# Performance work log

Measured on AMD Instinct MI355X. Metric: run time of the kernel, lower is better.

Reference implementation:

```python
import jax, jax.numpy as jnp
import numpy as np

N, E, B, H, L, T = 50000, 800000, 1000, 256, 5, 128
BN_EPS = 1e-5

def _bn(x, g, b):
    # training-mode batchnorm over node axis, biased variance (torch semantics)
    mu = jnp.mean(x, axis=0)
    var = jnp.mean(jnp.square(x - mu), axis=0)
    return (x - mu) * jax.lax.rsqrt(var + BN_EPS) * g + b

def setup_inputs() -> dict:
    key = jax.random.key(0)
    ks = jax.random.split(key, 12)
    s = lambda fan: 1.0 / np.sqrt(fan)
    inp = {}
    inp["x_atom"] = jax.random.normal(ks[0], (N, 9), jnp.float32)
    inp["x_pe"] = jax.random.normal(ks[1], (N, 8), jnp.float32)
    inp["edge_index"] = jax.random.randint(ks[2], (2, E), 0, N, dtype=jnp.int64)
    inp["batch"] = jnp.sort(jax.random.randint(ks[3], (N,), 0, B, dtype=jnp.int64))
    inp["ae_w"] = jax.random.normal(ks[4], (9, H), jnp.float32) * s(9)
    inp["ae_b"] = jnp.zeros((H,), jnp.float32)
    inp["pe_w"] = jax.random.normal(ks[5], (8, H), jnp.float32) * s(8)
    inp["pe_b"] = jnp.zeros((H,), jnp.float32)
    inp["w1"] = jax.random.normal(ks[6], (L, H, H), jnp.float32) * s(H)
    inp["b1"] = jnp.zeros((L, H), jnp.float32)
    inp["g1"] = jnp.ones((L, H), jnp.float32)
    inp["be1"] = jnp.zeros((L, H), jnp.float32)
    inp["w2"] = jax.random.normal(ks[7], (L, H, H), jnp.float32) * s(H)
    inp["b2"] = jnp.zeros((L, H), jnp.float32)
    inp["bng"] = jnp.ones((L, H), jnp.float32)
    inp["bnb"] = jnp.zeros((L, H), jnp.float32)
    inp["cl1_w"] = jax.random.normal(ks[8], (H, H), jnp.float32) * s(H)
    inp["cl1_b"] = jnp.zeros((H,), jnp.float32)
    inp["clg"] = jnp.ones((H,), jnp.float32)
    inp["clb"] = jnp.zeros((H,), jnp.float32)
    inp["cl2_w"] = jax.random.normal(ks[9], (H, T), jnp.float32) * s(H)
    inp["cl2_b"] = jnp.zeros((T,), jnp.float32)
    return inp

def reference(x_atom, x_pe, edge_index, batch, ae_w, ae_b, pe_w, pe_b,
              w1, b1, g1, be1, w2, b2, bng, bnb,
              cl1_w, cl1_b, clg, clb, cl2_w, cl2_b):
    src, dst = edge_index[0], edge_index[1]
    h = x_atom @ ae_w + ae_b + x_pe @ pe_w + pe_b  # (N, H)
    for i in range(L):
        # GINConv (eps=0): (1+eps)*x + sum_{j in N(i)} x_j, then MLP
        agg = jax.ops.segment_sum(h[src], dst, num_segments=N)
        z = h + agg
        z = z @ w1[i] + b1[i]
        z = jax.nn.relu(_bn(z, g1[i], be1[i]))
        z = z @ w2[i] + b2[i]
        # outer BN + ReLU (dropout is identity in eval)
        h = jax.nn.relu(_bn(z, bng[i], bnb[i]))
    # global mean pool per graph
    sums = jax.ops.segment_sum(h, batch, num_segments=B)
    counts = jax.ops.segment_sum(jnp.ones((N,), h.dtype), batch, num_segments=B)
    pooled = sums / jnp.maximum(counts, 1.0)[:, None]  # (B, H)
    z = pooled @ cl1_w + cl1_b
    z = jax.nn.relu(_bn(z, clg, clb))
    logits = z @ cl2_w + cl2_b  # (B, T)
    return logits
```

## Files before the change

kernel.cpp:

```cpp
#include <hip/hip_runtime.h>
#include <hip/hip_bf16.h>
#include <stdint.h>

#define HH 256
#define BN_EPS 1e-5f
#define CHUNK 256
#define NSLOT 12

static inline int cdiv(int a, int b) { return (a + b - 1) / b; }

typedef _Float16 f16x8 __attribute__((ext_vector_type(8)));
typedef __attribute__((ext_vector_type(4))) float f32x4;

__device__ __forceinline__ unsigned short f2h(float f) {
    _Float16 h = (_Float16)f;
    unsigned short u;
    __builtin_memcpy(&u, &h, 2);
    return u;
}
__device__ __forceinline__ float h2f(unsigned short u) {
    _Float16 h;
    __builtin_memcpy(&h, &u, 2);
    return (float)h;
}

__device__ __forceinline__ void gload16(const void* g, void* lds) {
    __builtin_amdgcn_global_load_lds((const __attribute__((address_space(1))) unsigned int*)g,
                                     (__attribute__((address_space(3))) unsigned int*)lds, 16, 0, 0);
}

__device__ __forceinline__ void bn_derive(const float* __restrict__ stats, const float* __restrict__ g,
                                          const float* __restrict__ b, float invM, int c,
                                          float& sc, float& sh) {
    float mu = stats[c] * invM;
    float var = stats[HH + c] * invM - mu * mu;
    float rstd = rsqrtf(var + BN_EPS);
    sc = rstd * g[c];
    sh = b[c] - mu * sc;
}

__global__ void embed_kernel(const float* __restrict__ xa, const float* __restrict__ xp,
                             const float* __restrict__ aw, const float* __restrict__ ab,
                             const float* __restrict__ pw, const float* __restrict__ pb,
                             unsigned short* __restrict__ h, int N) {
    int n = blockIdx.x;
    int c = threadIdx.x;
    if (n >= N) return;
    float acc = ab[c] + pb[c];
#pragma unroll
    for (int k = 0; k < 9; ++k) acc += xa[n * 9 + k] * aw[k * HH + c];
#pragma unroll
    for (int k = 0; k < 8; ++k) acc += xp[n * 8 + k] * pw[k * HH + c];
    h[(size_t)n * HH + c] = f2h(acc);
}

__global__ void zero_int_kernel(int* __restrict__ p, int n) {
    int i = blockIdx.x * blockDim.x + threadIdx.x;
    if (i < n) p[i] = 0;
}

__global__ void hist_kernel(const int* __restrict__ ei, int* __restrict__ deg, int E) {
    int e = blockIdx.x * blockDim.x + threadIdx.x;
    if (e < E) atomicAdd(&deg[ei[(size_t)E + e]], 1);
}

__global__ void ps1_kernel(const int* __restrict__ deg, int* __restrict__ chunkSum, int N) {
    __shared__ int sm[CHUNK];
    int i = blockIdx.x * CHUNK + threadIdx.x;
    sm[threadIdx.x] = (i < N) ? deg[i] : 0;
    __syncthreads();
    for (int off = CHUNK / 2; off > 0; off >>= 1) {
        if (threadIdx.x < off) sm[threadIdx.x] += sm[threadIdx.x + off];
        __syncthreads();
    }
    if (threadIdx.x == 0) chunkSum[blockIdx.x] = sm[0];
}

__global__ void ps2_kernel(const int* __restrict__ chunkSum, int* __restrict__ chunkOff,
                           int nc, int* __restrict__ offs, int N, int E) {
    __shared__ int sm[CHUNK];
    int t = threadIdx.x;
    int own = (t < nc) ? chunkSum[t] : 0;
    sm[t] = own;
    for (int off = 1; off < CHUNK; off <<= 1) {
        __syncthreads();
        int v = (t >= off) ? sm[t - off] : 0;
        __syncthreads();
        sm[t] += v;
    }
    if (t < nc) chunkOff[t] = sm[t] - own;
    if (t == 0) offs[N] = E;
}

__global__ void ps3_kernel(const int* __restrict__ deg, const int* __restrict__ chunkOff,
                           int* __restrict__ offs, int* __restrict__ cursor, int N) {
    __shared__ int sm[CHUNK];
    int t = threadIdx.x;
    int i = blockIdx.x * CHUNK + t;
    int own = (i < N) ? deg[i] : 0;
    sm[t] = own;
    for (int off = 1; off < CHUNK; off <<= 1) {
        __syncthreads();
        int v = (t >= off) ? sm[t - off] : 0;
        __syncthreads();
        sm[t] += v;
    }
    if (i < N) {
        int o = chunkOff[blockIdx.x] + sm[t] - own;
        offs[i] = o;
        cursor[i] = o;
    }
}

__global__ void fill_kernel(const int* __restrict__ ei, int* __restrict__ cursor,
                            int* __restrict__ srcl, int E) {
    int e = blockIdx.x * blockDim.x + threadIdx.x;
    if (e >= E) return;
    int s = ei[e];
    int d = ei[(size_t)E + e];
    int pos = atomicAdd(&cursor[d], 1);
    srcl[pos] = s;
}

__global__ void transpose_w_kernel(const float* __restrict__ W1, const float* __restrict__ W2,
                                   unsigned short* __restrict__ Wt1, unsigned short* __restrict__ Wt2,
                                   int perSet) {
    __shared__ float tile[32][33];
    int id = blockIdx.x;
    const float* W = W1;
    unsigned short* Wt = Wt1;
    if (id >= perSet) { W = W2; Wt = Wt2; id -= perSet; }
    int mat = id >> 6, t = id & 63;
    int kt = (t >> 3) * 32, nt = (t & 7) * 32;
    const float* Wm = W + (size_t)mat * HH * HH;
    unsigned short* Wtm = Wt + (size_t)mat * HH * HH;
    int lx = threadIdx.x & 31, ly = threadIdx.x >> 5;
#pragma unroll
    for (int yy = 0; yy < 32; yy += 8)
        tile[ly + yy][lx] = Wm[(size_t)(kt + ly + yy) * HH + nt + lx];
    __syncthreads();
#pragma unroll
    for (int yy = 0; yy < 32; yy += 8)
        Wtm[(size_t)(nt + ly + yy) * HH + kt + lx] = f2h(tile[lx][ly + yy]);
}

__global__ void init_stats_kernel(float* __restrict__ stats) {
    int i = blockIdx.x * blockDim.x + threadIdx.x;
    int slot = i >> 9;
    if (slot < NSLOT) stats[(size_t)slot * 4 * HH + (i & 511)] = 0.f;
}

__global__ __launch_bounds__(256) void aggregate_fused_kernel(
        const unsigned short* __restrict__ h,
        const int* __restrict__ offs, const int* __restrict__ srcl,
        const float* __restrict__ stats, const float* __restrict__ gv,
        const float* __restrict__ bv, float invM,
        unsigned short* __restrict__ z, int N) {
    int n = blockIdx.x * 4 + (threadIdx.x >> 6);
    int l = threadIdx.x & 63;
    if (n >= N) return;
    int c = l * 4;
    const bool apply = (stats != nullptr);
    float sc0 = 1.f, sc1 = 1.f, sc2 = 1.f, sc3 = 1.f;
    float sh0 = 0.f, sh1 = 0.f, sh2 = 0.f, sh3 = 0.f;
    if (apply) {
        bn_derive(stats, gv, bv, invM, c + 0, sc0, sh0);
        bn_derive(stats, gv, bv, invM, c + 1, sc1, sh1);
        bn_derive(stats, gv, bv, invM, c + 2, sc2, sh2);
        bn_derive(stats, gv, bv, invM, c + 3, sc3, sh3);
    }

#define LOADT(row, r0, r1, r2, r3)                                      \
    {                                                                   \
        ushort4 v_ = *(const ushort4*)&h[(size_t)(row) * HH + c];       \
        r0 = h2f(v_.x); r1 = h2f(v_.y); r2 = h2f(v_.z); r3 = h2f(v_.w); \
        if (apply) {                                                    \
            r0 = fmaxf(r0 * sc0 + sh0, 0.f);                            \
            r1 = fmaxf(r1 * sc1 + sh1, 0.f);                            \
            r2 = fmaxf(r2 * sc2 + sh2, 0.f);                            \
            r3 = fmaxf(r3 * sc3 + sh3, 0.f);                            \
        }                                                               \
    }

    float a0, a1, a2, a3;
    LOADT(n, a0, a1, a2, a3);
    int s0 = offs[n], s1 = offs[n + 1];
    int j = s0;
    for (; j + 4 <= s1; j += 4) {
        int r0 = srcl[j], r1 = srcl[j + 1], r2 = srcl[j + 2], r3 = srcl[j + 3];
        float t0, t1, t2, t3, u0, u1, u2, u3;
        float p0, p1, p2, p3, q0, q1, q2, q3;
        LOADT(r0, t0, t1, t2, t3);
        LOADT(r1, u0, u1, u2, u3);
        LOADT(r2, p0, p1, p2, p3);
        LOADT(r3, q0, q1, q2, q3);
        a0 += (t0 + u0) + (p0 + q0);
        a1 += (t1 + u1) + (p1 + q1);
        a2 += (t2 + u2) + (p2 + q2);
        a3 += (t3 + u3) + (p3 + q3);
    }
    for (; j < s1; ++j) {
        float t0, t1, t2, t3;
        LOADT(srcl[j], t0, t1, t2, t3);
        a0 += t0; a1 += t1; a2 += t2; a3 += t3;
    }
#undef LOADT
    ushort4 o;
    o.x = f2h(a0); o.y = f2h(a1); o.z = f2h(a2); o.w = f2h(a3);
    *(ushort4*)&z[(size_t)n * HH + c] = o;
}

template <bool BN>
__global__ __launch_bounds__(256) void mfma_gemm_t(const unsigned short* __restrict__ A,
                                                   const unsigned short* __restrict__ Wt,
                                                   const float* __restrict__ bias,
                                                   unsigned short* __restrict__ C,
                                                   float* __restrict__ stats,
                                                   const float* __restrict__ bnstats,
                                                   const float* __restrict__ gv,
                                                   const float* __restrict__ bv,
                                                   float invM, int M) {
    __shared__ unsigned short sm[128 * 136];
    __shared__ __align__(16) _Float16 lsc[256];
    __shared__ __align__(16) _Float16 lsh[256];
    unsigned short* As = sm;
    unsigned short* Bs = sm + 128 * 64;
    int tid = threadIdx.x;
    int w = tid >> 6, l = tid & 63;
    int wr = w >> 1, wc = w & 1;
    int row0 = blockIdx.y * 128;
    int col0 = blockIdx.x * 128;
    int g = (l & 7) ^ (l >> 3);
    int srow = w * 8 + (l >> 3);

    if (BN) {
        float sc, sh;
        bn_derive(bnstats, gv, bv, invM, tid, sc, sh);
        lsc[tid] = (_Float16)sc;
        lsh[tid] = (_Float16)sh;
        __syncthreads();
    }

    f32x4 acc[4][4] = {};

    const unsigned short* AB = A + (size_t)row0 * HH;
    const unsigned short* WB = Wt + (size_t)col0 * HH;

    for (int k0 = 0; k0 < 256; k0 += 64) {
#pragma unroll
        for (int r = 0; r < 4; ++r) {
            int row = r * 32 + srow;
            size_t go = (size_t)row * HH + k0 + g * 8;
            int lo = (r * 32 + w * 8) * 64;
            gload16(AB + go, &As[lo]);
            gload16(WB + go, &Bs[lo]);
        }
        __syncthreads();
#pragma unroll
        for (int kh = 0; kh < 2; ++kh) {
            f16x8 af[4], bf[4];
            f16x8 scv, shv;
            if (BN) {
                int kb = k0 + (kh * 4 + (l >> 4)) * 8;
                scv = *(const f16x8*)&lsc[kb];
                shv = *(const f16x8*)&lsh[kb];
            }
#pragma unroll
            for (int m = 0; m < 4; ++m) {
                int rr = wr * 64 + m * 16 + (l & 15);
                int gs = (kh * 4 + (l >> 4)) ^ (rr & 7);
                af[m] = *(const f16x8*)&As[rr * 64 + gs * 8];
                if (BN) {
                    af[m] = af[m] * scv + shv;
                    af[m] = __builtin_elementwise_max(af[m], (f16x8)(_Float16)0);
                }
            }
#pragma unroll
            for (int n = 0; n < 4; ++n) {
                int rr = wc * 64 + n * 16 + (l & 15);
                int gs = (kh * 4 + (l >> 4)) ^ (rr & 7);
                bf[n] = *(const f16x8*)&Bs[rr * 64 + gs * 8];
            }
#pragma unroll
            for (int m = 0; m < 4; ++m)
#pragma unroll
                for (int n = 0; n < 4; ++n)
                    acc[m][n] = __builtin_amdgcn_mfma_f32_16x16x32_f16(af[m], bf[n], acc[m][n], 0, 0, 0);
        }
        __syncthreads();
    }

    int mvalid = M - row0;
#pragma unroll
    for (int n = 0; n < 4; ++n) {
        int colr = wc * 64 + n * 16 + (l & 15);
        float bvv = bias[col0 + colr];
        float s = 0.f, s2 = 0.f;
#pragma unroll
        for (int m = 0; m < 4; ++m) {
            int rb = wr * 64 + m * 16 + (l >> 4) * 4;
#pragma unroll
            for (int r = 0; r < 4; ++r) {
                float v = acc[m][n][r] + bvv;
                sm[(rb + r) * 136 + colr] = f2h(v);
                if (rb + r < mvalid) { s += v; s2 += v * v; }
            }
        }
        s += __shfl_xor(s, 16);   s += __shfl_xor(s, 32);
        s2 += __shfl_xor(s2, 16); s2 += __shfl_xor(s2, 32);
        if ((l >> 4) == 0) {
            atomicAdd(&stats[col0 + colr], s);
            atomicAdd(&stats[HH + col0 + colr], s2);
        }
    }
    __syncthreads();
#pragma unroll
    for (int i = 0; i < 8; ++i) {
        int ci = i * 256 + tid;
        int row = ci >> 4;
        int cq = (ci & 15) * 8;
        if (row0 + row < M) {
            uint4 v = *(const uint4*)&sm[row * 136 + cq];
            *(uint4*)&C[(size_t)(row0 + row) * HH + col0 + cq] = v;
        }
    }
}

__global__ void bn_stats_kernel(const float* __restrict__ X, int M, float* __restrict__ stats) {
    int c = threadIdx.x;
    int r0 = blockIdx.x * 128;
    int r1 = min(r0 + 128, M);
    float s = 0.f, s2 = 0.f;
    for (int r = r0; r < r1; ++r) {
        float v = X[(size_t)r * HH + c];
        s += v;
        s2 += v * v;
    }
    atomicAdd(&stats[c], s);
    atomicAdd(&stats[HH + c], s2);
}

__global__ void bn_finalize_kernel(float* __restrict__ stats, const float* __restrict__ g,
                                   const float* __restrict__ b, float invM) {
    int c = threadIdx.x;
    float sc, sh;
    bn_derive(stats, g, b, invM, c, sc, sh);
    stats[2 * HH + c] = sc;
    stats[3 * HH + c] = sh;
}

__global__ void bn_apply_relu_kernel(float* __restrict__ X, int n4, const float* __restrict__ stats) {
    int i = blockIdx.x * blockDim.x + threadIdx.x;
    int stride = gridDim.x * blockDim.x;
    for (; i < n4; i += stride) {
        int c4 = (i & 63) * 4;
        float4 v = ((float4*)X)[i];
        float4 sc = *(const float4*)&stats[2 * HH + c4];
        float4 sh = *(const float4*)&stats[3 * HH + c4];
        v.x = fmaxf(v.x * sc.x + sh.x, 0.f);
        v.y = fmaxf(v.y * sc.y + sh.y, 0.f);
        v.z = fmaxf(v.z * sc.z + sh.z, 0.f);
        v.w = fmaxf(v.w * sc.w + sh.w, 0.f);
        ((float4*)X)[i] = v;
    }
}

__global__ __launch_bounds__(256) void gemm_kernel(const float* __restrict__ A,
                                                   const float* __restrict__ W,
                                                   const float* __restrict__ bias,
                                                   float* __restrict__ C,
                                                   int M, int ldw) {
    __shared__ float Asm[64][33];
    __shared__ float Wsm[32][64];
    int tid = threadIdx.x;
    int tx = tid & 15, ty = tid >> 4;
    int row0 = blockIdx.x * 64;
    int col0 = blockIdx.y * 64;
    float acc[4][4] = {};

    for (int k0 = 0; k0 < 256; k0 += 32) {
#pragma unroll
        for (int t = 0; t < 2; ++t) {
            int s = tid + t * 256;
            int m = s >> 3;
            int kq = (s & 7) * 4;
            float4 v = make_float4(0.f, 0.f, 0.f, 0.f);
            if (row0 + m < M) v = *(const float4*)&A[(size_t)(row0 + m) * 256 + k0 + kq];
            Asm[m][kq + 0] = v.x; Asm[m][kq + 1] = v.y; Asm[m][kq + 2] = v.z; Asm[m][kq + 3] = v.w;
        }
#pragma unroll
        for (int t = 0; t < 2; ++t) {
            int s = tid + t * 256;
            int kk = s >> 4;
            int cq = (s & 15) * 4;
            *(float4*)&Wsm[kk][cq] = *(const float4*)&W[(size_t)(k0 + kk) * ldw + col0 + cq];
        }
        __syncthreads();
#pragma unroll
        for (int kk = 0; kk < 32; ++kk) {
            float a0 = Asm[ty * 4 + 0][kk];
            float a1 = Asm[ty * 4 + 1][kk];
            float a2 = Asm[ty * 4 + 2][kk];
            float a3 = Asm[ty * 4 + 3][kk];
            float4 wv = *(const float4*)&Wsm[kk][tx * 4];
            acc[0][0] += a0 * wv.x; acc[0][1] += a0 * wv.y; acc[0][2] += a0 * wv.z; acc[0][3] += a0 * wv.w;
            acc[1][0] += a1 * wv.x; acc[1][1] += a1 * wv.y; acc[1][2] += a1 * wv.z; acc[1][3] += a1 * wv.w;
            acc[2][0] += a2 * wv.x; acc[2][1] += a2 * wv.y; acc[2][2] += a2 * wv.z; acc[2][3] += a2 * wv.w;
            acc[3][0] += a3 * wv.x; acc[3][1] += a3 * wv.y; acc[3][2] += a3 * wv.z; acc[3][3] += a3 * wv.w;
        }
        __syncthreads();
    }

    float4 bvv = *(const float4*)&bias[col0 + tx * 4];
#pragma unroll
    for (int j = 0; j < 4; ++j) {
        int row = row0 + ty * 4 + j;
        if (row < M) {
            float4 o = make_float4(acc[j][0] + bvv.x, acc[j][1] + bvv.y,
                                   acc[j][2] + bvv.z, acc[j][3] + bvv.w);
            *(float4*)&C[(size_t)row * ldw + col0 + tx * 4] = o;
        }
    }
}

__device__ __forceinline__ int lbound(const int* a, int n, int v) {
    int lo = 0, hi = n;
    while (lo < hi) {
        int mid = (lo + hi) >> 1;
        if (a[mid] < v) lo = mid + 1; else hi = mid;
    }
    return lo;
}

__global__ void pool_fused_kernel(const unsigned short* __restrict__ Hm,
                                  const int* __restrict__ batch,
                                  const float* __restrict__ stats,
                                  const float* __restrict__ gv,
                                  const float* __restrict__ bv, float invM,
                                  int N, float* __restrict__ pooled) {
    int g = blockIdx.x;
    int c = threadIdx.x;
    int s = lbound(batch, N, g);
    int e = lbound(batch, N, g + 1);
    float sc, sh;
    bn_derive(stats, gv, bv, invM, c, sc, sh);
    float acc = 0.f;
    for (int r = s; r < e; ++r)
        acc += fmaxf(h2f(Hm[(size_t)r * HH + c]) * sc + sh, 0.f);
    pooled[(size_t)g * HH + c] = acc / (float)max(e - s, 1);
}

extern "C" void kernel_launch(void* const* d_in, const int* in_sizes, int n_in,
                              void* d_out, int out_size, void* d_ws, size_t ws_size,
                              hipStream_t stream) {
    const float* x_atom = (const float*)d_in[0];
    const float* x_pe   = (const float*)d_in[1];
    const int* ei       = (const int*)d_in[2];
    const int* batch    = (const int*)d_in[3];
    const float* ae_w = (const float*)d_in[4];
    const float* ae_b = (const float*)d_in[5];
    const float* pe_w = (const float*)d_in[6];
    const float* pe_b = (const float*)d_in[7];
    const float* w1  = (const float*)d_in[8];
    const float* b1  = (const float*)d_in[9];
    const float* g1  = (const float*)d_in[10];
    const float* be1 = (const float*)d_in[11];
    const float* w2  = (const float*)d_in[12];
    const float* b2  = (const float*)d_in[13];
    const float* bng = (const float*)d_in[14];
    const float* bnb = (const float*)d_in[15];
    const float* cl1_w = (const float*)d_in[16];
    const float* cl1_b = (const float*)d_in[17];
    const float* clg = (const float*)d_in[18];
    const float* clb = (const float*)d_in[19];
    const float* cl2_w = (const float*)d_in[20];
    const float* cl2_b = (const float*)d_in[21];

    const int N = in_sizes[3];
    const int E = in_sizes[2] / 2;
    const int T = in_sizes[21];
    const int B = out_size / T;
    const int Lnum = in_sizes[9] / HH;
    const int nc = cdiv(N, CHUNK);
    const int Npad = cdiv(N, 128) * 128;
    const size_t P = (size_t)Npad * HH;

    unsigned short* X = (unsigned short*)d_ws;
    unsigned short* Y = X + P;
    unsigned short* wt1 = Y + P;
    unsigned short* wt2 = wt1 + (size_t)Lnum * HH * HH;
    float* stats = (float*)(wt2 + (size_t)Lnum * HH * HH);
    float* pooled = stats + (size_t)NSLOT * 4 * HH;
    float* zc = pooled + (size_t)B * HH;
    int* deg = (int*)(zc + (size_t)B * HH);
    int* offs = deg + N;
    int* cursor = offs + N + 1;
    int* chunkSum = cursor + N;
    int* chunkOff = chunkSum + 256;
    int* srcl = chunkOff + 256;

    const int BH4 = B * (HH / 4);
    const float invN = 1.f / (float)N;

    zero_int_kernel<<<cdiv(N, 256), 256, 0, stream>>>(deg, N);
    hist_kernel<<<cdiv(E, 256), 256, 0, stream>>>(ei, deg, E);
    ps1_kernel<<<nc, CHUNK, 0, stream>>>(deg, chunkSum, N);
    ps2_kernel<<<1, CHUNK, 0, stream>>>(chunkSum, chunkOff, nc, offs, N, E);
    ps3_kernel<<<nc, CHUNK, 0, stream>>>(deg, chunkOff, offs, cursor, N);
    fill_kernel<<<cdiv(E, 256), 256, 0, stream>>>(ei, cursor, srcl, E);

    transpose_w_kernel<<<2 * Lnum * 64, 256, 0, stream>>>(w1, w2, wt1, wt2, Lnum * 64);

    init_stats_kernel<<<cdiv(NSLOT * 512, 256), 256, 0, stream>>>(stats);

    embed_kernel<<<N, HH, 0, stream>>>(x_atom, x_pe, ae_w, ae_b, pe_w, pe_b, X, N);

    dim3 mf_grid(2, cdiv(N, 128));

    unsigned short *in = X, *ot = Y;

    for (int i = 0; i < Lnum; ++i) {
        float* slot1 = stats + (size_t)(2 * i) * 4 * HH;
        float* slot2 = stats + (size_t)(2 * i + 1) * 4 * HH;
        const float* aggStats = (i == 0) ? nullptr : stats + (size_t)(2 * i - 1) * 4 * HH;
        const float* aggG = (i == 0) ? nullptr : bng + (size_t)(i - 1) * HH;
        const float* aggB = (i == 0) ? nullptr : bnb + (size_t)(i - 1) * HH;

        aggregate_fused_kernel<<<cdiv(N, 4), 256, 0, stream>>>(in, offs, srcl,
                                                               aggStats, aggG, aggB, invN, ot, N);

        mfma_gemm_t<false><<<mf_grid, 256, 0, stream>>>(ot, wt1 + (size_t)i * HH * HH,
                                                        b1 + (size_t)i * HH, in, slot1,
                                                        nullptr, nullptr, nullptr, 0.f, N);

        mfma_gemm_t<true><<<mf_grid, 256, 0, stream>>>(in, wt2 + (size_t)i * HH * HH,
                                                       b2 + (size_t)i * HH, ot, slot2,
                                                       slot1, g1 + (size_t)i * HH,
                                                       be1 + (size_t)i * HH, invN, N);

        unsigned short* t = in; in = ot; ot = t;
    }

    pool_fused_kernel<<<B, HH, 0, stream>>>(in, batch,
                                            stats + (size_t)(2 * Lnum - 1) * 4 * HH,
                                            bng + (size_t)(Lnum - 1) * HH,
                                            bnb + (size_t)(Lnum - 1) * HH, invN, N, pooled);

    float* slotC = stats + (size_t)10 * 4 * HH;
    dim3 cls_grid1(cdiv(B, 64), HH / 64);
    gemm_kernel<<<cls_grid1, 256, 0, stream>>>(pooled, cl1_w, cl1_b, zc, B, HH);
    bn_stats_kernel<<<cdiv(B, 128), HH, 0, stream>>>(zc, B, slotC);
    bn_finalize_kernel<<<1, HH, 0, stream>>>(slotC, clg, clb, 1.f / B);
    bn_apply_relu_kernel<<<min(2048, cdiv(BH4, 256)), 256, 0, stream>>>(zc, BH4, slotC);

    dim3 cls_grid2(cdiv(B, 64), T / 64);
    gemm_kernel<<<cls_grid2, 256, 0, stream>>>(zc, cl2_w, cl2_b, (float*)d_out, B, T);
}
```

Before: 1.018 ms.

## Remap GEMM block order for XCD locality, pre-reduce BN stats in LDS, merge init kernels

Result: faster. 888.6 us (-12.7%).

```diff
diff --git a/kernel.cpp b/kernel.cpp
--- a/kernel.cpp
+++ b/kernel.cpp
@@ -54,9 +54,13 @@
     h[(size_t)n * HH + c] = f2h(acc);
 }
 
-__global__ void zero_int_kernel(int* __restrict__ p, int n) {
+__global__ void setup_kernel(int* __restrict__ deg, int N, float* __restrict__ stats) {
     int i = blockIdx.x * blockDim.x + threadIdx.x;
-    if (i < n) p[i] = 0;
+    if (i < N) deg[i] = 0;
+    if (i < NSLOT * 512) {
+        int slot = i >> 9;
+        stats[(size_t)slot * 4 * HH + (i & 511)] = 0.f;
+    }
 }
 
 __global__ void hist_kernel(const int* __restrict__ ei, int* __restrict__ deg, int E) {
@@ -142,12 +146,6 @@
 #pragma unroll
     for (int yy = 0; yy < 32; yy += 8)
         Wtm[(size_t)(nt + ly + yy) * HH + kt + lx] = f2h(tile[lx][ly + yy]);
-}
-
-__global__ void init_stats_kernel(float* __restrict__ stats) {
-    int i = blockIdx.x * blockDim.x + threadIdx.x;
-    int slot = i >> 9;
-    if (slot < NSLOT) stats[(size_t)slot * 4 * HH + (i & 511)] = 0.f;
 }
 
 __global__ __launch_bounds__(256) void aggregate_fused_kernel(
@@ -223,13 +221,29 @@
     __shared__ unsigned short sm[128 * 136];
     __shared__ __align__(16) _Float16 lsc[256];
     __shared__ __align__(16) _Float16 lsh[256];
+    __shared__ float sred[256];
     unsigned short* As = sm;
     unsigned short* Bs = sm + 128 * 64;
     int tid = threadIdx.x;
     int w = tid >> 6, l = tid & 63;
     int wr = w >> 1, wc = w & 1;
-    int row0 = blockIdx.y * 128;
-    int col0 = blockIdx.x * 128;
+
+    int nRow = (M + 127) >> 7;
+    int fullIds = (nRow & ~7) * 2;
+    int id = blockIdx.x;
+    int p, cc;
+    if (id < fullIds) {
+        int gq = id >> 4, r = id & 15;
+        cc = r >> 3;
+        p = gq * 8 + (r & 7);
+    } else {
+        int t = id - fullIds;
+        p = (nRow & ~7) + (t >> 1);
+        cc = t & 1;
+    }
+    int row0 = p * 128;
+    int col0 = cc * 128;
+
     int g = (l & 7) ^ (l >> 3);
     int srow = w * 8 + (l >> 3);
 
@@ -291,6 +305,7 @@
     }
 
     int mvalid = M - row0;
+    float sv[4], s2v[4];
 #pragma unroll
     for (int n = 0; n < 4; ++n) {
         int colr = wc * 64 + n * 16 + (l & 15);
@@ -308,12 +323,26 @@
         }
         s += __shfl_xor(s, 16);   s += __shfl_xor(s, 32);
         s2 += __shfl_xor(s2, 16); s2 += __shfl_xor(s2, 32);
-        if ((l >> 4) == 0) {
-            atomicAdd(&stats[col0 + colr], s);
-            atomicAdd(&stats[HH + col0 + colr], s2);
+        sv[n] = s;
+        s2v[n] = s2;
+    }
+    if (wr == 1 && (l >> 4) == 0) {
+#pragma unroll
+        for (int n = 0; n < 4; ++n) {
+            int colr = wc * 64 + n * 16 + (l & 15);
+            sred[colr] = sv[n];
+            sred[128 + colr] = s2v[n];
         }
     }
     __syncthreads();
+    if (wr == 0 && (l >> 4) == 0) {
+#pragma unroll
+        for (int n = 0; n < 4; ++n) {
+            int colr = wc * 64 + n * 16 + (l & 15);
+            atomicAdd(&stats[col0 + colr], sv[n] + sred[colr]);
+            atomicAdd(&stats[HH + col0 + colr], s2v[n] + sred[128 + colr]);
+        }
+    }
 #pragma unroll
     for (int i = 0; i < 8; ++i) {
         int ci = i * 256 + tid;
@@ -502,7 +531,8 @@
     const int BH4 = B * (HH / 4);
     const float invN = 1.f / (float)N;
 
-    zero_int_kernel<<<cdiv(N, 256), 256, 0, stream>>>(deg, N);
+    setup_kernel<<<cdiv(max(N, NSLOT * 512), 256), 256, 0, stream>>>(deg, N, stats);
+
     hist_kernel<<<cdiv(E, 256), 256, 0, stream>>>(ei, deg, E);
     ps1_kernel<<<nc, CHUNK, 0, stream>>>(deg, chunkSum, N);
     ps2_kernel<<<1, CHUNK, 0, stream>>>(chunkSum, chunkOff, nc, offs, N, E);
@@ -511,11 +541,10 @@
 
     transpose_w_kernel<<<2 * Lnum * 64, 256, 0, stream>>>(w1, w2, wt1, wt2, Lnum * 64);
 
-    init_stats_kernel<<<cdiv(NSLOT * 512, 256), 256, 0, stream>>>(stats);
-
     embed_kernel<<<N, HH, 0, stream>>>(x_atom, x_pe, ae_w, ae_b, pe_w, pe_b, X, N);
 
-    dim3 mf_grid(2, cdiv(N, 128));
+    const int nRow = cdiv(N, 128);
+    const int mf_blocks = 2 * nRow;
 
     unsigned short *in = X, *ot = Y;
 
@@ -529,14 +558,14 @@
         aggregate_fused_kernel<<<cdiv(N, 4), 256, 0, stream>>>(in, offs, srcl,
                                                                aggStats, aggG, aggB, invN, ot, N);
 
-        mfma_gemm_t<false><<<mf_grid, 256, 0, stream>>>(ot, wt1 + (size_t)i * HH * HH,
-                                                        b1 + (size_t)i * HH, in, slot1,
-                                                        nullptr, nullptr, nullptr, 0.f, N);
-
-        mfma_gemm_t<true><<<mf_grid, 256, 0, stream>>>(in, wt2 + (size_t)i * HH * HH,
-                                                       b2 + (size_t)i * HH, ot, slot2,
-                                                       slot1, g1 + (size_t)i * HH,
-                                                       be1 + (size_t)i * HH, invN, N);
+        mfma_gemm_t<false><<<mf_blocks, 256, 0, stream>>>(ot, wt1 + (size_t)i * HH * HH,
+                                                          b1 + (size_t)i * HH, in, slot1,
+                                                          nullptr, nullptr, nullptr, 0.f, N);
+
+        mfma_gemm_t<true><<<mf_blocks, 256, 0, stream>>>(in, wt2 + (size_t)i * HH * HH,
+                                                         b2 + (size_t)i * HH, ot, slot2,
+                                                         slot1, g1 + (size_t)i * HH,
+                                                         be1 + (size_t)i * HH, invN, N);
 
         unsigned short* t = in; in = ot; ot = t;
     }
```
